# Performance work log

Measured on AMD Instinct MI355X. Metric: run time of the kernel, lower is better.

The kernel has to match this reference:

```python
import jax, jax.numpy as jnp
import numpy as np

E = 8          # num_experts
K = 2          # top-k experts per token
CAP_RATIO = 1.05


def setup_inputs() -> dict:
    key = jax.random.key(0)
    k0, k1, k2, k3 = jax.random.split(key, 4)
    B, S, D, H = 2, 2048, 512, 2048
    return {
        "x": jax.random.normal(k0, (B, S, D), jnp.float32),
        "gate_w": jax.random.normal(k1, (E, D), jnp.float32) * (1.0 / np.sqrt(D)),
        "fc1_w": jax.random.normal(k2, (E, D, H), jnp.float32) * (1.0 / np.sqrt(D)),
        "fc1_b": jnp.zeros((E, H), jnp.float32),
        "fc2_w": jax.random.normal(k3, (E, H, D), jnp.float32) * (1.0 / np.sqrt(H)),
        "fc2_b": jnp.zeros((E, D), jnp.float32),
    }


def reference(x, gate_w, fc1_w, fc1_b, fc2_w, fc2_b):
    B, S, D = x.shape
    xf = x.reshape(-1, D)               # [T, D]
    T = xf.shape[0]

    # ---- router (eval mode: no noise) ----
    logits = xf @ gate_w.T              # [T, E]
    gates = jax.nn.softmax(logits, axis=-1)
    top_g, top_i = jax.lax.top_k(gates, K)   # [T, K]

    # importance auxiliary loss (std unbiased=False == jnp.std default)
    imp = gates.sum(axis=0)                  # [E]
    imp_loss = (jnp.std(imp) / (imp.mean() + 1e-6)) ** 2

    # ---- capacity-limited dispatch mask ----
    # torch loops slot-major: slot 0 over all tokens in order, then slot 1.
    # position of each (slot, token) entry within its expert's queue:
    buffer_cap = round(K * T * CAP_RATIO / E)
    idx_sm = top_i.T.reshape(-1)                        # [K*T] slot-major
    oh = jax.nn.one_hot(idx_sm, E, dtype=jnp.int32)     # [K*T, E]
    pos = jnp.cumsum(oh, axis=0) - oh                   # earlier same-expert count
    pos_e = jnp.take_along_axis(pos, idx_sm[:, None], axis=1)[:, 0]
    within = (pos_e < buffer_cap).reshape(K, T).T       # [T, K] bool

    wf = within.astype(xf.dtype)
    oh_tke = jax.nn.one_hot(top_i, E, dtype=xf.dtype) * wf[..., None]  # dispatch mask [T,K,E]
    combine_te = jnp.einsum('tk,tke->te', top_g * wf, oh_tke / jnp.maximum(oh_tke, 1e-30) * oh_tke) if False else jnp.einsum('tk,tke->te', top_g * wf, jax.nn.one_hot(top_i, E, dtype=xf.dtype))

    # load-balance loss from post-capacity token counts
    tokens_per_expert = oh_tke.sum(axis=(0, 1))         # [E]
    l_load = (jnp.std(tokens_per_expert) / (tokens_per_expert.mean() + 1e-6)) ** 2
    l_aux = 0.5 * (imp_loss + l_load)

    # ---- per-expert MLP (dense compute, masked combine) ----
    h = jnp.einsum('td,edh->teh', xf, fc1_w) + fc1_b[None]      # [T, E, H]
    h = jax.nn.gelu(h, approximate=False)                       # torch nn.GELU default
    y = jnp.einsum('teh,ehd->ted', h, fc2_w) + fc2_b[None]      # [T, E, D]

    out = jnp.einsum('te,ted->td', combine_te, y).reshape(B, S, D)
    return out, l_aux, l_load
```

## Files before the change

kernel.cpp:

```cpp
#include <hip/hip_runtime.h>
#include <hip/hip_bf16.h>

#define E_    8
#define TT    4096
#define DD    512
#define HH    2048
#define CAP   1075
#define MPAD  1152
#define MT    9
#define MT2   18

typedef __bf16 bf16_t;
typedef bf16_t bf16x4 __attribute__((ext_vector_type(4)));
typedef bf16_t bf16x8 __attribute__((ext_vector_type(8)));
typedef float  f32x4  __attribute__((ext_vector_type(4)));
typedef unsigned int u32;

__device__ __forceinline__ bf16_t tobf(float f) { return (bf16_t)f; }

__device__ __forceinline__ float gelu_f(float v) {
  const float u = v * (0.7978845608028654f + 0.035677408136300125f * v * v);
  const float a = __builtin_fabsf(u);
  const float ex = __expf(2.0f * a);
  float th = 1.0f - 2.0f / (ex + 1.0f);
  th = __builtin_copysignf(th, u);
  return 0.5f * v * (1.0f + th);
}

#define OFF_TOPI  256u
#define OFF_TOPG  (OFF_TOPI + 4096u*2u*4u)
#define OFF_SLOT  (OFF_TOPG + 4096u*2u*4u)
#define OFF_ETOK  (OFF_SLOT + 4096u*2u*4u)
#define OFF_EWT   (OFF_ETOK + 8u*1152u*4u)
#define OFF_XG    (OFF_EWT  + 8u*1152u*4u)
#define XG_BYTES  (8u*1152u*512u*2u)
#define OFF_W1T   (OFF_XG + XG_BYTES)
#define W1T_BYTES (8u*512u*2048u*2u)
#define OFF_W2T   (OFF_W1T + W1T_BYTES)
#define W2T_BYTES (8u*2048u*512u*2u)
#define OFF_H     (OFF_W2T + W2T_BYTES)
#define H_BYTES   (8u*1152u*2048u*2u)
#define OFF_Y     OFF_XG

__global__ __launch_bounds__(256) void router_kernel(
    const float* __restrict__ x, const float* __restrict__ gw,
    float* __restrict__ imp, int* __restrict__ top_i, float* __restrict__ top_g) {
  const int tid = threadIdx.x;
  const int wid = tid >> 6, lane = tid & 63;
  const int t = blockIdx.x * 4 + wid;

  float p[E_];
#pragma unroll
  for (int e = 0; e < E_; ++e) p[e] = 0.f;
  const float* xr = x + (size_t)t * DD;
#pragma unroll
  for (int it = 0; it < DD / 64; ++it) {
    const int d = it * 64 + lane;
    const float xv = xr[d];
#pragma unroll
    for (int e = 0; e < E_; ++e) p[e] += xv * gw[e * DD + d];
  }
#pragma unroll
  for (int off = 32; off > 0; off >>= 1) {
#pragma unroll
    for (int e = 0; e < E_; ++e) p[e] += __shfl_down(p[e], off);
  }

  __shared__ float simp[4][E_];
  if (lane == 0) {
    float mx = p[0];
#pragma unroll
    for (int e = 1; e < E_; ++e) mx = fmaxf(mx, p[e]);
    float g[E_]; float s = 0.f;
#pragma unroll
    for (int e = 0; e < E_; ++e) { g[e] = expf(p[e] - mx); s += g[e]; }
    const float inv = 1.f / s;
#pragma unroll
    for (int e = 0; e < E_; ++e) { g[e] *= inv; simp[wid][e] = g[e]; }
    int i0 = 0;
#pragma unroll
    for (int e = 1; e < E_; ++e) if (g[e] > g[i0]) i0 = e;
    int i1 = (i0 == 0) ? 1 : 0;
#pragma unroll
    for (int e = 0; e < E_; ++e) if (e != i0 && g[e] > g[i1]) i1 = e;
    top_i[t * 2 + 0] = i0;  top_i[t * 2 + 1] = i1;
    top_g[t * 2 + 0] = g[i0]; top_g[t * 2 + 1] = g[i1];
  }
  __syncthreads();
  if (tid < E_) {
    const float s = simp[0][tid] + simp[1][tid] + simp[2][tid] + simp[3][tid];
    atomicAdd(&imp[tid], s);
  }
}

__global__ __launch_bounds__(1024) void capacity_kernel(
    const int* __restrict__ top_i, const float* __restrict__ top_g,
    const float* __restrict__ imp, int* __restrict__ etok, float* __restrict__ ewt,
    int* __restrict__ slot_map, int* __restrict__ kept, float* __restrict__ scal) {
  __shared__ u32 wt[16][4];
  const int tid = threadIdx.x, wave = tid >> 6, lane = tid & 63;

  int eidx[8];
#pragma unroll
  for (int q = 0; q < 8; ++q) {
    const int j = tid * 8 + q;
    const int k = j >> 12, t = j & (TT - 1);
    eidx[q] = top_i[t * 2 + k];
  }
  u32 pk[4] = {0u, 0u, 0u, 0u};
#pragma unroll
  for (int q = 0; q < 8; ++q) pk[eidx[q] >> 1] += 1u << ((eidx[q] & 1) * 16);

  u32 v[4] = {pk[0], pk[1], pk[2], pk[3]};
#pragma unroll
  for (int off = 1; off < 64; off <<= 1) {
#pragma unroll
    for (int p = 0; p < 4; ++p) {
      const u32 n = (u32)__shfl_up((int)v[p], off);
      if (lane >= off) v[p] += n;
    }
  }
  if (lane == 63) {
#pragma unroll
    for (int p = 0; p < 4; ++p) wt[wave][p] = v[p];
  }
  __syncthreads();
  u32 base[4] = {0u, 0u, 0u, 0u}, tot[4] = {0u, 0u, 0u, 0u};
#pragma unroll
  for (int w = 0; w < 16; ++w) {
#pragma unroll
    for (int p = 0; p < 4; ++p) {
      const u32 xv = wt[w][p];
      if (w < wave) base[p] += xv;
      tot[p] += xv;
    }
  }
  int run[E_];
#pragma unroll
  for (int p = 0; p < 4; ++p) {
    const u32 excl = base[p] + v[p] - pk[p];
    run[2 * p]     = (int)(excl & 0xFFFFu);
    run[2 * p + 1] = (int)(excl >> 16);
  }
#pragma unroll
  for (int q = 0; q < 8; ++q) {
    const int e = eidx[q];
    const int pos = run[e]++;
    const int j = tid * 8 + q;
    if (pos < CAP) {
      const int k = j >> 12, t = j & (TT - 1);
      etok[e * MPAD + pos] = t;
      ewt[e * MPAD + pos] = top_g[t * 2 + k];
      slot_map[j] = (e << 16) | pos;
    } else {
      slot_map[j] = -1;
    }
  }
  if (tid == 0) {
    float tpe[E_];
#pragma unroll
    for (int p = 0; p < 4; ++p) {
      const int t0 = (int)(tot[p] & 0xFFFFu), t1 = (int)(tot[p] >> 16);
      const int k0 = t0 < CAP ? t0 : CAP, k1 = t1 < CAP ? t1 : CAP;
      kept[2 * p] = k0; kept[2 * p + 1] = k1;
      tpe[2 * p] = (float)k0; tpe[2 * p + 1] = (float)k1;
    }
    float ms = 0.f;
#pragma unroll
    for (int e = 0; e < E_; ++e) ms += tpe[e];
    ms *= (1.f / E_);
    float vt = 0.f;
#pragma unroll
    for (int e = 0; e < E_; ++e) { const float d = tpe[e] - ms; vt += d * d; }
    vt *= (1.f / E_);
    const float ll = vt / ((ms + 1e-6f) * (ms + 1e-6f));

    float iv[E_], mi = 0.f;
#pragma unroll
    for (int e = 0; e < E_; ++e) { iv[e] = imp[e]; mi += iv[e]; }
    mi *= (1.f / E_);
    float vi = 0.f;
#pragma unroll
    for (int e = 0; e < E_; ++e) { const float d = iv[e] - mi; vi += d * d; }
    vi *= (1.f / E_);
    const float il = vi / ((mi + 1e-6f) * (mi + 1e-6f));

    scal[0] = 0.5f * (il + ll);
    scal[1] = ll;
  }
}

__global__ __launch_bounds__(256) void gather_kernel(
    const float* __restrict__ x, const int* __restrict__ etok,
    const int* __restrict__ kept, bf16_t* __restrict__ Xg) {
  const int e = blockIdx.y, wid = threadIdx.x >> 6, lane = threadIdx.x & 63;
  const int m = blockIdx.x * 4 + wid;
  if (m >= kept[e]) return;
  const int t = etok[e * MPAD + m];
  const float* src = x + (size_t)t * DD + lane * 8;
  const float4 a = *(const float4*)src;
  const float4 b = *(const float4*)(src + 4);
  bf16_t tmp[8] = {tobf(a.x), tobf(a.y), tobf(a.z), tobf(a.w),
                   tobf(b.x), tobf(b.y), tobf(b.z), tobf(b.w)};
  *(bf16x8*)(Xg + ((size_t)e * MPAD + m) * DD + lane * 8) = *(const bf16x8*)tmp;
}

__global__ __launch_bounds__(256) void transpose_both_kernel(
    const float* __restrict__ fc1, bf16_t* __restrict__ w1t,
    const float* __restrict__ fc2, bf16_t* __restrict__ w2t) {
  __shared__ float tile[64][65];
  const int z = blockIdx.z;
  const bool first = (z < 8);
  const int e = first ? z : z - 8;
  const int R = first ? DD : HH;
  const int C = first ? HH : DD;
  const int ct = first ? blockIdx.x : blockIdx.y;
  const int rt = first ? blockIdx.y : blockIdx.x;
  const float* ip = (first ? fc1 : fc2) + (size_t)e * DD * HH;
  bf16_t* op = (first ? w1t : w2t) + (size_t)e * DD * HH;
  const int r0 = rt * 64, c0 = ct * 64;
  const int tid = threadIdx.x;
  const int rr = tid >> 6, cc = tid & 63;
#pragma unroll
  for (int p = 0; p < 16; ++p)
    tile[p * 4 + rr][cc] = ip[(size_t)(r0 + p * 4 + rr) * C + c0 + cc];
  __syncthreads();
  const int g = tid & 15, ob = tid >> 4;
#pragma unroll
  for (int p = 0; p < 4; ++p) {
    const int oc = p * 16 + ob;
    bf16x4 o4;
    o4.x = tobf(tile[g * 4 + 0][oc]);
    o4.y = tobf(tile[g * 4 + 1][oc]);
    o4.z = tobf(tile[g * 4 + 2][oc]);
    o4.w = tobf(tile[g * 4 + 3][oc]);
    *(bf16x4*)(op + (size_t)(c0 + oc) * R + r0 + g * 4) = o4;
  }
}

template <int MI, int KLEN, int KSTR>
__device__ __forceinline__ void gemm_core(
    const bf16_t* __restrict__ A, const bf16_t* __restrict__ B,
    bf16_t* As, bf16_t* Bs, f32x4 (&acc)[4][MI]) {
  const int tid = threadIdx.x;
  const int wave = tid >> 6, lane = tid & 63;
  const int r8 = lane >> 3;
  const int kswz = ((lane & 7) ^ r8) * 8;
  const bf16_t* ga = A + (size_t)(wave * (MI * 8) + r8) * KSTR + kswz;
  const bf16_t* gb = B + (size_t)(wave * 32 + r8) * KSTR + kswz;
  const int mw = (wave >> 1) * (MI * 16), nw = (wave & 1) * 64;
  const int l15 = lane & 15, quad = lane >> 4;
  const int sw = l15 & 7;

  for (int k0 = 0; k0 < KLEN; k0 += 64) {
    __syncthreads();
#pragma unroll
    for (int p = 0; p < MI; ++p) {
      __builtin_amdgcn_global_load_lds(
          (const __attribute__((address_space(1))) void*)(ga + (size_t)p * 8 * KSTR + k0),
          (__attribute__((address_space(3))) void*)(As + (wave * (MI * 8) + p * 8) * 64),
          16, 0, 0);
    }
#pragma unroll
    for (int p = 0; p < 4; ++p) {
      __builtin_amdgcn_global_load_lds(
          (const __attribute__((address_space(1))) void*)(gb + (size_t)p * 8 * KSTR + k0),
          (__attribute__((address_space(3))) void*)(Bs + (wave * 32 + p * 8) * 64),
          16, 0, 0);
    }
    __syncthreads();
#pragma unroll
    for (int ks = 0; ks < 2; ++ks) {
      bf16x8 af[MI], bfr[4];
#pragma unroll
      for (int i = 0; i < MI; ++i)
        af[i] = *(const bf16x8*)(As + (mw + i * 16 + l15) * 64 + (((ks * 4 + quad) ^ sw) << 3));
#pragma unroll
      for (int j = 0; j < 4; ++j)
        bfr[j] = *(const bf16x8*)(Bs + (nw + j * 16 + l15) * 64 + (((ks * 4 + quad) ^ sw) << 3));
#pragma unroll
      for (int j = 0; j < 4; ++j)
#pragma unroll
        for (int i = 0; i < MI; ++i)
          acc[j][i] = __builtin_amdgcn_mfma_f32_16x16x32_bf16(bfr[j], af[i], acc[j][i], 0, 0, 0);
    }
  }
}

__global__ __launch_bounds__(256, 4) void gemm1_kernel(
    const bf16_t* __restrict__ Xg, const bf16_t* __restrict__ W1t,
    const float* __restrict__ b1, bf16_t* __restrict__ Hbuf) {
  __shared__ __align__(16) bf16_t As[128 * 64];
  __shared__ __align__(16) bf16_t Bs[128 * 64];
  const int e = blockIdx.x, tileN = blockIdx.y, tileM = blockIdx.z;
  const bf16_t* A = Xg + ((size_t)e * MPAD + tileM * 128) * DD;
  const bf16_t* B = W1t + ((size_t)e * HH + tileN * 128) * DD;
  f32x4 acc[4][4];
  const f32x4 z = {0.f, 0.f, 0.f, 0.f};
#pragma unroll
  for (int j = 0; j < 4; ++j)
#pragma unroll
    for (int i = 0; i < 4; ++i) acc[j][i] = z;
  gemm_core<4, DD, DD>(A, B, As, Bs, acc);

  const int tid = threadIdx.x, wave = tid >> 6, lane = tid & 63;
  const int mw = (wave >> 1) * 64, nw = (wave & 1) * 64;
  const int l15 = lane & 15, quad = lane >> 4;
#pragma unroll
  for (int j = 0; j < 4; ++j) {
    const int n0 = tileN * 128 + nw + j * 16 + quad * 4;
    const float4 b4 = *(const float4*)(b1 + e * HH + n0);
#pragma unroll
    for (int i = 0; i < 4; ++i) {
      const int m = tileM * 128 + mw + i * 16 + l15;
      bf16x4 h4;
      h4.x = tobf(gelu_f(acc[j][i][0] + b4.x));
      h4.y = tobf(gelu_f(acc[j][i][1] + b4.y));
      h4.z = tobf(gelu_f(acc[j][i][2] + b4.z));
      h4.w = tobf(gelu_f(acc[j][i][3] + b4.w));
      *(bf16x4*)(Hbuf + ((size_t)e * MPAD + m) * HH + n0) = h4;
    }
  }
}

__global__ __launch_bounds__(256, 6) void gemm2_kernel(
    const bf16_t* __restrict__ Hbuf, const bf16_t* __restrict__ W2t,
    const int* __restrict__ kept, bf16_t* __restrict__ Ybuf) {
  __shared__ __align__(16) bf16_t As[64 * 64];
  __shared__ __align__(16) bf16_t Bs[128 * 64];
  const int e = blockIdx.x, tileN = blockIdx.y, tileM = blockIdx.z;
  const bf16_t* A = Hbuf + ((size_t)e * MPAD + tileM * 64) * HH;
  const bf16_t* B = W2t + ((size_t)e * DD + tileN * 128) * HH;
  f32x4 acc[4][2];
  const f32x4 z = {0.f, 0.f, 0.f, 0.f};
#pragma unroll
  for (int j = 0; j < 4; ++j)
#pragma unroll
    for (int i = 0; i < 2; ++i) acc[j][i] = z;
  gemm_core<2, HH, HH>(A, B, As, Bs, acc);

  const int tid = threadIdx.x, wave = tid >> 6, lane = tid & 63;
  const int mw = (wave >> 1) * 32, nw = (wave & 1) * 64;
  const int l15 = lane & 15, quad = lane >> 4;
  const int nk = kept[e];
#pragma unroll
  for (int j = 0; j < 4; ++j) {
    const int n0 = tileN * 128 + nw + j * 16 + quad * 4;
#pragma unroll
    for (int i = 0; i < 2; ++i) {
      const int m = tileM * 64 + mw + i * 16 + l15;
      if (m < nk) {
        bf16x4 o4;
        o4.x = tobf(acc[j][i][0]);
        o4.y = tobf(acc[j][i][1]);
        o4.z = tobf(acc[j][i][2]);
        o4.w = tobf(acc[j][i][3]);
        *(bf16x4*)(Ybuf + ((size_t)e * MPAD + m) * DD + n0) = o4;
      }
    }
  }
}

__global__ __launch_bounds__(128) void combine_kernel(
    const bf16_t* __restrict__ Ybuf, const float* __restrict__ b2,
    const int* __restrict__ slot_map, const float* __restrict__ top_g,
    float* __restrict__ out) {
  const int t = blockIdx.x;
  const int c = threadIdx.x * 4;
  float4 acc = {0.f, 0.f, 0.f, 0.f};
#pragma unroll
  for (int k = 0; k < 2; ++k) {
    const int sm = slot_map[k * TT + t];
    if (sm >= 0) {
      const int e = sm >> 16, pos = sm & 0xFFFF;
      const float w = top_g[t * 2 + k];
      const bf16x4 y4 = *(const bf16x4*)(Ybuf + ((size_t)e * MPAD + pos) * DD + c);
      const float4 bb = *(const float4*)(b2 + e * DD + c);
      acc.x += w * ((float)y4.x + bb.x);
      acc.y += w * ((float)y4.y + bb.y);
      acc.z += w * ((float)y4.z + bb.z);
      acc.w += w * ((float)y4.w + bb.w);
    }
  }
  *(float4*)(out + (size_t)t * DD + c) = acc;
}

extern "C" void kernel_launch(void* const* d_in, const int* in_sizes, int n_in,
                              void* d_out, int out_size, void* d_ws, size_t ws_size,
                              hipStream_t stream) {
  const float* x      = (const float*)d_in[0];
  const float* gate_w = (const float*)d_in[1];
  const float* fc1_w  = (const float*)d_in[2];
  const float* fc1_b  = (const float*)d_in[3];
  const float* fc2_w  = (const float*)d_in[4];
  const float* fc2_b  = (const float*)d_in[5];
  float* out = (float*)d_out;

  char* ws = (char*)d_ws;
  float*  imp   = (float*)(ws + 0);
  int*    kept  = (int*)(ws + 64);
  int*    top_i = (int*)(ws + OFF_TOPI);
  float*  top_g = (float*)(ws + OFF_TOPG);
  int*    slotm = (int*)(ws + OFF_SLOT);
  int*    etok  = (int*)(ws + OFF_ETOK);
  float*  ewt   = (float*)(ws + OFF_EWT);
  bf16_t* Xg    = (bf16_t*)(ws + OFF_XG);
  bf16_t* W1t   = (bf16_t*)(ws + OFF_W1T);
  bf16_t* W2t   = (bf16_t*)(ws + OFF_W2T);
  bf16_t* Hbuf  = (bf16_t*)(ws + OFF_H);
  bf16_t* Ybuf  = (bf16_t*)(ws + OFF_Y);
  float*  scal  = out + (size_t)TT * DD;

  hipMemsetAsync(ws, 0, 256, stream);

  transpose_both_kernel<<<dim3(32, 8, 16), 256, 0, stream>>>(fc1_w, W1t, fc2_w, W2t);

  router_kernel<<<TT / 4, 256, 0, stream>>>(x, gate_w, imp, top_i, top_g);
  capacity_kernel<<<1, 1024, 0, stream>>>(top_i, top_g, imp, etok, ewt, slotm, kept, scal);
  gather_kernel<<<dim3(MPAD / 4, E_), 256, 0, stream>>>(x, etok, kept, Xg);

  gemm1_kernel<<<dim3(E_, HH / 128, MT), 256, 0, stream>>>(Xg, W1t, fc1_b, Hbuf);
  gemm2_kernel<<<dim3(E_, DD / 128, MT2), 256, 0, stream>>>(Hbuf, W2t, kept, Ybuf);
  combine_kernel<<<TT, 128, 0, stream>>>(Ybuf, fc2_b, slotm, top_g, out);
}
```

Before: 228.6 us.

## Double-buffer B tiles in LDS and load A fragments directly from global

The shared GEMM core now keeps two LDS buffers for the B (weight) tile. It prefetches the next K-slice with global_load_lds while the current slice is consumed, which leaves a single barrier per iteration. The A operand no longer goes through LDS: each lane loads its MFMA fragments straight from global memory. The aim is to hide global latency behind MFMA work and reduce barrier and LDS traffic. The costs are duplicate A loads between the waves that share rows, and uncoalesced, latency-exposed A reads. The compiler may also insert conservative vmcnt waits that serialise the prefetch. The gemm2 occupancy hint drops from 6 to 5.

```diff
diff --git a/kernel.cpp b/kernel.cpp
--- a/kernel.cpp
+++ b/kernel.cpp
@@ -9,6 +9,7 @@
 #define MPAD  1152
 #define MT    9
 #define MT2   18
+#define BTILE (128 * 64)
 
 typedef __bf16 bf16_t;
 typedef bf16_t bf16x4 __attribute__((ext_vector_type(4)));
@@ -241,48 +242,57 @@
 template <int MI, int KLEN, int KSTR>
 __device__ __forceinline__ void gemm_core(
     const bf16_t* __restrict__ A, const bf16_t* __restrict__ B,
-    bf16_t* As, bf16_t* Bs, f32x4 (&acc)[4][MI]) {
+    bf16_t* Bs, f32x4 (&acc)[4][MI]) {
   const int tid = threadIdx.x;
   const int wave = tid >> 6, lane = tid & 63;
   const int r8 = lane >> 3;
   const int kswz = ((lane & 7) ^ r8) * 8;
-  const bf16_t* ga = A + (size_t)(wave * (MI * 8) + r8) * KSTR + kswz;
   const bf16_t* gb = B + (size_t)(wave * 32 + r8) * KSTR + kswz;
   const int mw = (wave >> 1) * (MI * 16), nw = (wave & 1) * 64;
   const int l15 = lane & 15, quad = lane >> 4;
   const int sw = l15 & 7;
+  const bf16_t* ga = A + (size_t)(mw + l15) * KSTR + quad * 8;
+
+#pragma unroll
+  for (int p = 0; p < 4; ++p) {
+    __builtin_amdgcn_global_load_lds(
+        (const __attribute__((address_space(1))) void*)(gb + (size_t)p * 8 * KSTR),
+        (__attribute__((address_space(3))) void*)(Bs + (wave * 32 + p * 8) * 64),
+        16, 0, 0);
+  }
 
   for (int k0 = 0; k0 < KLEN; k0 += 64) {
+    const int cur = (k0 >> 6) & 1;
     __syncthreads();
-#pragma unroll
-    for (int p = 0; p < MI; ++p) {
-      __builtin_amdgcn_global_load_lds(
-          (const __attribute__((address_space(1))) void*)(ga + (size_t)p * 8 * KSTR + k0),
-          (__attribute__((address_space(3))) void*)(As + (wave * (MI * 8) + p * 8) * 64),
-          16, 0, 0);
-    }
-#pragma unroll
-    for (int p = 0; p < 4; ++p) {
-      __builtin_amdgcn_global_load_lds(
-          (const __attribute__((address_space(1))) void*)(gb + (size_t)p * 8 * KSTR + k0),
-          (__attribute__((address_space(3))) void*)(Bs + (wave * 32 + p * 8) * 64),
-          16, 0, 0);
-    }
-    __syncthreads();
+    if (k0 + 64 < KLEN) {
+      bf16_t* bnx = Bs + (cur ^ 1) * BTILE;
+#pragma unroll
+      for (int p = 0; p < 4; ++p) {
+        __builtin_amdgcn_global_load_lds(
+            (const __attribute__((address_space(1))) void*)(gb + (size_t)p * 8 * KSTR + k0 + 64),
+            (__attribute__((address_space(3))) void*)(bnx + (wave * 32 + p * 8) * 64),
+            16, 0, 0);
+      }
+    }
+    bf16x8 af[2][MI];
+#pragma unroll
+    for (int ks = 0; ks < 2; ++ks)
+#pragma unroll
+      for (int i = 0; i < MI; ++i)
+        af[ks][i] = *(const bf16x8*)(ga + (size_t)i * 16 * KSTR + k0 + ks * 32);
+
+    const bf16_t* bc = Bs + cur * BTILE;
 #pragma unroll
     for (int ks = 0; ks < 2; ++ks) {
-      bf16x8 af[MI], bfr[4];
-#pragma unroll
-      for (int i = 0; i < MI; ++i)
-        af[i] = *(const bf16x8*)(As + (mw + i * 16 + l15) * 64 + (((ks * 4 + quad) ^ sw) << 3));
+      bf16x8 bfr[4];
 #pragma unroll
       for (int j = 0; j < 4; ++j)
-        bfr[j] = *(const bf16x8*)(Bs + (nw + j * 16 + l15) * 64 + (((ks * 4 + quad) ^ sw) << 3));
+        bfr[j] = *(const bf16x8*)(bc + (nw + j * 16 + l15) * 64 + (((ks * 4 + quad) ^ sw) << 3));
 #pragma unroll
       for (int j = 0; j < 4; ++j)
 #pragma unroll
         for (int i = 0; i < MI; ++i)
-          acc[j][i] = __builtin_amdgcn_mfma_f32_16x16x32_bf16(bfr[j], af[i], acc[j][i], 0, 0, 0);
+          acc[j][i] = __builtin_amdgcn_mfma_f32_16x16x32_bf16(bfr[j], af[ks][i], acc[j][i], 0, 0, 0);
     }
   }
 }
@@ -290,8 +300,7 @@
 __global__ __launch_bounds__(256, 4) void gemm1_kernel(
     const bf16_t* __restrict__ Xg, const bf16_t* __restrict__ W1t,
     const float* __restrict__ b1, bf16_t* __restrict__ Hbuf) {
-  __shared__ __align__(16) bf16_t As[128 * 64];
-  __shared__ __align__(16) bf16_t Bs[128 * 64];
+  __shared__ __align__(16) bf16_t Bs[2 * BTILE];
   const int e = blockIdx.x, tileN = blockIdx.y, tileM = blockIdx.z;
   const bf16_t* A = Xg + ((size_t)e * MPAD + tileM * 128) * DD;
   const bf16_t* B = W1t + ((size_t)e * HH + tileN * 128) * DD;
@@ -301,7 +310,7 @@
   for (int j = 0; j < 4; ++j)
 #pragma unroll
     for (int i = 0; i < 4; ++i) acc[j][i] = z;
-  gemm_core<4, DD, DD>(A, B, As, Bs, acc);
+  gemm_core<4, DD, DD>(A, B, Bs, acc);
 
   const int tid = threadIdx.x, wave = tid >> 6, lane = tid & 63;
   const int mw = (wave >> 1) * 64, nw = (wave & 1) * 64;
@@ -323,11 +332,10 @@
   }
 }
 
-__global__ __launch_bounds__(256, 6) void gemm2_kernel(
+__global__ __launch_bounds__(256, 5) void gemm2_kernel(
     const bf16_t* __restrict__ Hbuf, const bf16_t* __restrict__ W2t,
     const int* __restrict__ kept, bf16_t* __restrict__ Ybuf) {
-  __shared__ __align__(16) bf16_t As[64 * 64];
-  __shared__ __align__(16) bf16_t Bs[128 * 64];
+  __shared__ __align__(16) bf16_t Bs[2 * BTILE];
   const int e = blockIdx.x, tileN = blockIdx.y, tileM = blockIdx.z;
   const bf16_t* A = Hbuf + ((size_t)e * MPAD + tileM * 64) * HH;
   const bf16_t* B = W2t + ((size_t)e * DD + tileN * 128) * HH;
@@ -337,7 +345,7 @@
   for (int j = 0; j < 4; ++j)
 #pragma unroll
     for (int i = 0; i < 2; ++i) acc[j][i] = z;
-  gemm_core<2, HH, HH>(A, B, As, Bs, acc);
+  gemm_core<2, HH, HH>(A, B, Bs, acc);
 
   const int tid = threadIdx.x, wave = tid >> 6, lane = tid & 63;
   const int mw = (wave >> 1) * 32, nw = (wave & 1) * 64;
```

New measurement: 280.8 us. +22.8%, slower.
